# Performance work log

Measured on AMD Instinct MI355X. Metric: run time of the kernel, lower is better.

The kernel has to match this reference:

```python
import jax, jax.numpy as jnp
import numpy as np

NUM_CLASSES = 80
NUM_MASKED = 3
SCALE_XY = 1.2
STRIDE = 8.0
# yolov4 anchors for mask [0,1,2], divided by stride
_ANCHORS = np.array([[12.0, 16.0], [19.0, 36.0], [40.0, 28.0]], dtype=np.float32) / STRIDE


def setup_inputs() -> dict:
    key = jax.random.key(0)
    x = jax.random.normal(key, (16, NUM_MASKED * (5 + NUM_CLASSES), 76, 76), dtype=jnp.float32)
    return {"x": x}


def reference(x):
    B, C, H, W = x.shape
    A, nc, s = NUM_MASKED, NUM_CLASSES, SCALE_XY
    anchors = jnp.asarray(_ANCHORS)  # [A, 2]
    o = x.reshape(B, A, 5 + nc, H, W)
    # yolov4 (new_coords==0) transforms
    bxy = jax.nn.sigmoid(o[:, :, 0:2]) * s - 0.5 * (s - 1.0)  # [B,A,2,H,W]
    bwh = jnp.exp(o[:, :, 2:4])                               # [B,A,2,H,W]
    det = jax.nn.sigmoid(o[:, :, 4])                          # [B,A,H,W]
    cls = jax.nn.sigmoid(o[:, :, 5:])                         # [B,A,nc,H,W]
    grid_x = jnp.arange(W, dtype=x.dtype)                     # broadcasts over W
    grid_y = jnp.arange(H, dtype=x.dtype)[:, None]            # broadcasts over H
    bx = (bxy[:, :, 0] + grid_x) / W
    by = (bxy[:, :, 1] + grid_y) / H
    bw = bwh[:, :, 0] * anchors[None, :, 0, None, None] / W
    bh = bwh[:, :, 1] * anchors[None, :, 1, None, None] / H
    bx1 = bx - bw * 0.5
    by1 = by - bh * 0.5
    bx2 = bx - bw * 0.5 + bw
    by2 = by - bh * 0.5 + bh
    boxes = jnp.stack((bx1, by1, bx2, by2), axis=-1).reshape(B, A * H * W, 4)
    # cls [B,A,nc,H,W] -> [B,A,H,W,nc], scaled by objectness
    confs = (cls * det[:, :, None]).transpose(0, 1, 3, 4, 2).reshape(B, A * H * W, nc)
    return jnp.concatenate([boxes, confs], axis=-1)  # [B, A*H*W, 4+nc]
```

## Files before the change

kernel.cpp:

```cpp
#include <hip/hip_runtime.h>


#define YHW 5776
#define W76 76
#define NROWS 4
#define NRB 19
#define LSTRIDE 77
#define NTHREADS 512
#define QN 19
#define NQ (85 * QN)
#define NJ 4

typedef float f4v __attribute__((ext_vector_type(4)));

__device__ __forceinline__ float fsigmoid(float v) {
    return __builtin_amdgcn_rcpf(1.0f + __expf(-v));
}

__device__ __forceinline__ void issue_loads(const float* __restrict__ src, int toff,
                                            f4v r[NJ], int tid) {
    #pragma unroll
    for (int j = 0; j < NJ; ++j) {
        const int idx = tid + NTHREADS * j;
        if (idx < NQ) {
            const int ch = idx / QN;
            const int q  = idx - ch * QN;
            r[j] = *reinterpret_cast<const f4v*>(src + (size_t)ch * YHW + 4 * q + toff);
        }
    }
}

__device__ __forceinline__ void transform(const f4v r[NJ], float (*lds)[LSTRIDE], int tid) {
    #pragma unroll
    for (int j = 0; j < NJ; ++j) {
        const int idx = tid + NTHREADS * j;
        if (idx < NQ) {
            const int ch = idx / QN;
            const int q  = idx - ch * QN;
            f4v v = r[j];
            int row;
            if (ch < 2) {
                v.x = fsigmoid(v.x) * 1.2f - 0.1f;
                v.y = fsigmoid(v.y) * 1.2f - 0.1f;
                v.z = fsigmoid(v.z) * 1.2f - 0.1f;
                v.w = fsigmoid(v.w) * 1.2f - 0.1f;
                row = ch;
            } else if (ch < 4) {
                v.x = __expf(v.x); v.y = __expf(v.y);
                v.z = __expf(v.z); v.w = __expf(v.w);
                row = ch;
            } else {
                v.x = fsigmoid(v.x); v.y = fsigmoid(v.y);
                v.z = fsigmoid(v.z); v.w = fsigmoid(v.w);
                row = (ch == 4) ? 84 : ch - 1;
            }
            const int p4 = 4 * q;
            lds[row][p4 + 0] = v.x;
            lds[row][p4 + 1] = v.y;
            lds[row][p4 + 2] = v.z;
            lds[row][p4 + 3] = v.w;
        }
    }
}

__device__ __forceinline__ void drain(const float (*lds)[LSTRIDE], float* __restrict__ dst,
                                      int h, float ax, float ay, int tid) {
    const float inv = 1.0f / 76.0f;
    constexpr int total = W76 * 21;
    #pragma unroll
    for (int u0 = 0; u0 < total; u0 += NTHREADS) {
        const int u = u0 + tid;
        if (u < total) {
            const int pp = u / 21;
            const int c  = u - 21 * pp;
            f4v o;
            if (c == 0) {
                const float sx = lds[0][pp];
                const float sy = lds[1][pp];
                const float ew = lds[2][pp];
                const float eh = lds[3][pp];
                const float bxc = (sx + (float)pp) * inv;
                const float byc = (sy + (float)h) * inv;
                const float bw  = ew * ax * inv;
                const float bh  = eh * ay * inv;
                const float bx1 = bxc - 0.5f * bw;
                const float by1 = byc - 0.5f * bh;
                o.x = bx1; o.y = by1; o.z = bx1 + bw; o.w = by1 + bh;
            } else {
                const float det = lds[84][pp];
                o.x = lds[4 * c + 0][pp] * det;
                o.y = lds[4 * c + 1][pp] * det;
                o.z = lds[4 * c + 2][pp] * det;
                o.w = lds[4 * c + 3][pp] * det;
            }
            *reinterpret_cast<f4v*>(dst + (size_t)pp * 84 + 4 * c) = o;
        }
    }
}

__global__ __launch_bounds__(NTHREADS) void yolo_kernel(const float* __restrict__ x,
                                                        float* __restrict__ out) {
    const int blk  = blockIdx.x;
    const int rb   = blk % NRB;
    const int ba   = blk / NRB;
    const int a    = ba % 3;
    const int row0 = rb * NROWS;

    __shared__ float lds[85][LSTRIDE];

    const int tid = threadIdx.x;
    const float* __restrict__ srcbase = x + (size_t)ba * 85 * YHW + (size_t)row0 * W76;
    float* __restrict__ dstbase = out + ((size_t)ba * YHW + (size_t)row0 * W76) * 84;

    const float ax = (a == 0) ? 1.5f : ((a == 1) ? 2.375f : 5.0f);
    const float ay = (a == 0) ? 2.0f : ((a == 1) ? 4.5f : 3.5f);

    f4v rA[NJ], rB[NJ];
    issue_loads(srcbase, 0, rA, tid);

#define STEP(T, CUR, NXT, ISLAST)                                              \
    transform(CUR, lds, tid);                                                  \
    __syncthreads();                                                           \
    if (!(ISLAST)) issue_loads(srcbase, ((T) + 1) * W76, NXT, tid);            \
    drain(lds, dstbase + (size_t)(T) * W76 * 84, row0 + (T), ax, ay, tid);     \
    if (!(ISLAST)) __syncthreads();

    STEP(0, rA, rB, 0)
    STEP(1, rB, rA, 0)
    STEP(2, rA, rB, 0)
    STEP(3, rB, rA, 1)
#undef STEP
}

extern "C" void kernel_launch(void* const* d_in, const int* in_sizes, int n_in,
                              void* d_out, int out_size, void* d_ws, size_t ws_size,
                              hipStream_t stream) {
    const float* x = (const float*)d_in[0];
    float* out = (float*)d_out;
    const int nblocks = 48 * NRB;
    yolo_kernel<<<nblocks, NTHREADS, 0, stream>>>(x, out);
}
```

Baseline: 37.89 us.

## Halve rows per block, clamp tail indices, and pin prefetch ahead of drain

Each block now handles 2 rows instead of 4, so the grid doubles to 1824 blocks. The out-of-range guard in the load and transform loops is replaced by clamping the index to the last valid element, which removes divergent branches. Surplus threads redundantly recompute and rewrite the same final LDS slot. A sched_barrier keeps the next-row prefetch issued before the drain, and the per-block pipeline shrinks to two steps, trading fewer rows of load/store overlap per block for more blocks in flight.

Result: no change. 37.93 us (+0.1%).

```diff
diff --git a/kernel.cpp b/kernel.cpp
--- a/kernel.cpp
+++ b/kernel.cpp
@@ -3,8 +3,8 @@
 
 #define YHW 5776
 #define W76 76
-#define NROWS 4
-#define NRB 19
+#define NROWS 2
+#define NRB 38
 #define LSTRIDE 77
 #define NTHREADS 512
 #define QN 19
@@ -21,45 +21,43 @@
                                             f4v r[NJ], int tid) {
     #pragma unroll
     for (int j = 0; j < NJ; ++j) {
-        const int idx = tid + NTHREADS * j;
-        if (idx < NQ) {
-            const int ch = idx / QN;
-            const int q  = idx - ch * QN;
-            r[j] = *reinterpret_cast<const f4v*>(src + (size_t)ch * YHW + 4 * q + toff);
-        }
+        int idx = tid + NTHREADS * j;
+        idx = (idx < NQ) ? idx : (NQ - 1);
+        const int ch = idx / QN;
+        const int q  = idx - ch * QN;
+        r[j] = *reinterpret_cast<const f4v*>(src + (size_t)ch * YHW + 4 * q + toff);
     }
 }
 
 __device__ __forceinline__ void transform(const f4v r[NJ], float (*lds)[LSTRIDE], int tid) {
     #pragma unroll
     for (int j = 0; j < NJ; ++j) {
-        const int idx = tid + NTHREADS * j;
-        if (idx < NQ) {
-            const int ch = idx / QN;
-            const int q  = idx - ch * QN;
-            f4v v = r[j];
-            int row;
-            if (ch < 2) {
-                v.x = fsigmoid(v.x) * 1.2f - 0.1f;
-                v.y = fsigmoid(v.y) * 1.2f - 0.1f;
-                v.z = fsigmoid(v.z) * 1.2f - 0.1f;
-                v.w = fsigmoid(v.w) * 1.2f - 0.1f;
-                row = ch;
-            } else if (ch < 4) {
-                v.x = __expf(v.x); v.y = __expf(v.y);
-                v.z = __expf(v.z); v.w = __expf(v.w);
-                row = ch;
-            } else {
-                v.x = fsigmoid(v.x); v.y = fsigmoid(v.y);
-                v.z = fsigmoid(v.z); v.w = fsigmoid(v.w);
-                row = (ch == 4) ? 84 : ch - 1;
-            }
-            const int p4 = 4 * q;
-            lds[row][p4 + 0] = v.x;
-            lds[row][p4 + 1] = v.y;
-            lds[row][p4 + 2] = v.z;
-            lds[row][p4 + 3] = v.w;
+        int idx = tid + NTHREADS * j;
+        idx = (idx < NQ) ? idx : (NQ - 1);
+        const int ch = idx / QN;
+        const int q  = idx - ch * QN;
+        f4v v = r[j];
+        int row;
+        if (ch < 2) {
+            v.x = fsigmoid(v.x) * 1.2f - 0.1f;
+            v.y = fsigmoid(v.y) * 1.2f - 0.1f;
+            v.z = fsigmoid(v.z) * 1.2f - 0.1f;
+            v.w = fsigmoid(v.w) * 1.2f - 0.1f;
+            row = ch;
+        } else if (ch < 4) {
+            v.x = __expf(v.x); v.y = __expf(v.y);
+            v.z = __expf(v.z); v.w = __expf(v.w);
+            row = ch;
+        } else {
+            v.x = fsigmoid(v.x); v.y = fsigmoid(v.y);
+            v.z = fsigmoid(v.z); v.w = fsigmoid(v.w);
+            row = (ch == 4) ? 84 : ch - 1;
         }
+        const int p4 = 4 * q;
+        lds[row][p4 + 0] = v.x;
+        lds[row][p4 + 1] = v.y;
+        lds[row][p4 + 2] = v.z;
+        lds[row][p4 + 3] = v.w;
     }
 }
 
@@ -118,18 +116,16 @@
     f4v rA[NJ], rB[NJ];
     issue_loads(srcbase, 0, rA, tid);
 
-#define STEP(T, CUR, NXT, ISLAST)                                              \
-    transform(CUR, lds, tid);                                                  \
-    __syncthreads();                                                           \
-    if (!(ISLAST)) issue_loads(srcbase, ((T) + 1) * W76, NXT, tid);            \
-    drain(lds, dstbase + (size_t)(T) * W76 * 84, row0 + (T), ax, ay, tid);     \
-    if (!(ISLAST)) __syncthreads();
+    transform(rA, lds, tid);
+    __syncthreads();
+    issue_loads(srcbase, W76, rB, tid);
+    __builtin_amdgcn_sched_barrier(0);
+    drain(lds, dstbase, row0, ax, ay, tid);
+    __syncthreads();
 
-    STEP(0, rA, rB, 0)
-    STEP(1, rB, rA, 0)
-    STEP(2, rA, rB, 0)
-    STEP(3, rB, rA, 1)
-#undef STEP
+    transform(rB, lds, tid);
+    __syncthreads();
+    drain(lds, dstbase + (size_t)W76 * 84, row0 + 1, ax, ay, tid);
 }
 
 extern "C" void kernel_launch(void* const* d_in, const int* in_sizes, int n_in,
```
